# Performance work log

Hardware: AMD Instinct MI355X
Metric: run time of the kernel (lower is better)

The kernel has to match this reference:

```python
import jax, jax.numpy as jnp
import numpy as np

EMBED = 256
HEADS = 8
LEVELS = 4
POINTS = 8
HD = EMBED // HEADS  # 32


def setup_inputs() -> dict:
    key = jax.random.key(0)
    ks = jax.random.split(key, 12)
    bs, nq = 1, 22500
    shapes = np.array([[100, 100], [50, 50], [25, 25], [13, 13]], dtype=np.int32)
    areas = shapes[:, 0] * shapes[:, 1]
    nv = int(areas.sum())  # 13294
    lsi = np.concatenate([[0], np.cumsum(areas)[:-1]]).astype(np.int32)
    s = 1.0 / np.sqrt(EMBED)
    return {
        "query": jax.random.normal(ks[0], (bs, nq, EMBED), jnp.float32),
        "value": jax.random.normal(ks[1], (bs, nv, EMBED), jnp.float32),
        "reference_points": jax.random.uniform(ks[2], (bs, nq, LEVELS, 2), jnp.float32),
        "spatial_shapes": shapes,          # static int metadata
        "level_start_index": lsi,          # static int metadata
        "W_value": jax.random.normal(ks[3], (EMBED, EMBED), jnp.float32) * s,
        "b_value": jax.random.normal(ks[4], (EMBED,), jnp.float32) * 0.01,
        "W_off": jax.random.normal(ks[5], (EMBED, HEADS * LEVELS * POINTS * 2), jnp.float32) * s,
        "b_off": jax.random.normal(ks[6], (HEADS * LEVELS * POINTS * 2,), jnp.float32) * 0.5,
        "W_attn": jax.random.normal(ks[7], (EMBED, HEADS * LEVELS * POINTS), jnp.float32) * s,
        "b_attn": jax.random.normal(ks[8], (HEADS * LEVELS * POINTS,), jnp.float32) * 0.01,
        "W_out": jax.random.normal(ks[9], (EMBED, EMBED), jnp.float32) * s,
        "b_out": jax.random.normal(ks[10], (EMBED,), jnp.float32) * 0.01,
    }


def _bilinear(img, xy):
    # img: (B, H, W, C); xy: (B, N, 2) normalized to [0,1], align_corners=False,
    # zero padding for out-of-range samples (matches F.grid_sample in the torch fallback).
    B, H, W, C = img.shape
    x = xy[..., 0] * W - 0.5
    y = xy[..., 1] * H - 0.5
    x0f = jnp.floor(x)
    y0f = jnp.floor(y)
    wx = (x - x0f)[..., None]
    wy = (y - y0f)[..., None]
    x0 = x0f.astype(jnp.int32)
    y0 = y0f.astype(jnp.int32)
    flat = img.reshape(B, H * W, C)

    def g(yi, xi):
        valid = ((yi >= 0) & (yi < H) & (xi >= 0) & (xi < W)).astype(img.dtype)
        idx = jnp.clip(yi, 0, H - 1) * W + jnp.clip(xi, 0, W - 1)
        return jnp.take_along_axis(flat, idx[..., None], axis=1) * valid[..., None]

    v00 = g(y0, x0)
    v01 = g(y0, x0 + 1)
    v10 = g(y0 + 1, x0)
    v11 = g(y0 + 1, x0 + 1)
    return (v00 * (1 - wy) * (1 - wx) + v01 * (1 - wy) * wx
            + v10 * wy * (1 - wx) + v11 * wy * wx)


def reference(query, value, reference_points, spatial_shapes, level_start_index,
              W_value, b_value, W_off, b_off, W_attn, b_attn, W_out, b_out):
    bs, nq, _ = query.shape
    # value projection -> per-head values (bs, nv, H, hd)
    v = (value @ W_value + b_value).reshape(bs, -1, HEADS, HD)
    # sampling offsets (bs, nq, H, L, P, 2) and attention weights softmaxed over L*P
    off = (query @ W_off + b_off).reshape(bs, nq, HEADS, LEVELS, POINTS, 2)
    aw = jax.nn.softmax((query @ W_attn + b_attn).reshape(bs, nq, HEADS, LEVELS * POINTS), -1)
    aw = aw.reshape(bs, nq, HEADS, LEVELS, POINTS)
    ss = np.asarray(spatial_shapes)
    norm = jnp.asarray(np.stack([ss[:, 1], ss[:, 0]], -1).astype(np.float32))  # (L, 2) as (W, H)
    loc = reference_points[:, :, None, :, None, :] + off / norm[None, None, None, :, None, :]
    out = jnp.zeros((bs, nq, HEADS, HD), query.dtype)
    start = 0
    for l in range(LEVELS):
        H, W = int(ss[l, 0]), int(ss[l, 1])
        vl = v[:, start:start + H * W].reshape(bs, H, W, HEADS, HD)
        vl = vl.transpose(0, 3, 1, 2, 4).reshape(bs * HEADS, H, W, HD)
        ll = loc[:, :, :, l].transpose(0, 2, 1, 3, 4).reshape(bs * HEADS, nq * POINTS, 2)
        samp = _bilinear(vl, ll).reshape(bs, HEADS, nq, POINTS, HD)
        out = out + jnp.einsum('bhqp,bhqpd->bqhd', aw[:, :, :, l].transpose(0, 2, 1, 3), samp)
        start += H * W
    out = out.reshape(bs, nq, EMBED) @ W_out + b_out
    return query + out  # identity residual (identity defaults to query)
```

## Files before the change

### kernel.cpp

```cpp
#include <hip/hip_runtime.h>
#include <hip/hip_bf16.h>
#include <cstdint>

#define NQ 22500
#define NV 13294
#define EMBED 256

typedef short bf16x8 __attribute__((ext_vector_type(8)));
typedef float f32x4  __attribute__((ext_vector_type(4)));

__device__ __forceinline__ int lvlH(int l) { return l==0?100 : l==1?50 : l==2?25 : 13; }
__device__ __forceinline__ int lvlW(int l) { return l==0?100 : l==1?50 : l==2?25 : 13; }
__device__ __forceinline__ int lvlStart(int l) { return l==0?0 : l==1?10000 : l==2?12500 : 13125; }

__device__ __forceinline__ ushort f2bf(float x) {
    uint32_t u = __float_as_uint(x);
    uint32_t r = (u + 0x7FFFu + ((u >> 16) & 1u)) >> 16;
    return (ushort)r;
}

__global__ __launch_bounds__(256) void prep_kernel(
    const float* __restrict__ value, const float* __restrict__ query,
    const float* __restrict__ Wv, const float* __restrict__ Wo,
    const float* __restrict__ Wa, const float* __restrict__ Wt,
    ushort* __restrict__ val_bf, ushort* __restrict__ q_bf,
    ushort* __restrict__ Wv_t, ushort* __restrict__ Wo_t,
    ushort* __restrict__ Wa_t, ushort* __restrict__ Wt_t)
{
    const int y = blockIdx.y;
    const int idx0 = blockIdx.x * 256 + threadIdx.x;
    const int stride = gridDim.x * 256;

    if (y == 0) {
        for (int i = idx0; i < (NV * 256) / 4; i += stride) {
            float4 v = ((const float4*)value)[i];
            ushort4 o; o.x = f2bf(v.x); o.y = f2bf(v.y); o.z = f2bf(v.z); o.w = f2bf(v.w);
            ((ushort4*)val_bf)[i] = o;
        }
    } else if (y == 1) {
        for (int i = idx0; i < (NQ * 256) / 4; i += stride) {
            float4 v = ((const float4*)query)[i];
            ushort4 o; o.x = f2bf(v.x); o.y = f2bf(v.y); o.z = f2bf(v.z); o.w = f2bf(v.w);
            ((ushort4*)q_bf)[i] = o;
        }
    } else if (y == 2) {
        for (int i = idx0; i < 256 * 256; i += stride) {
            int n = i & 255, k = i >> 8;
            Wv_t[n * 256 + k] = f2bf(Wv[k * 256 + n]);
        }
    } else if (y == 3) {
        for (int i = idx0; i < 512 * 256; i += stride) {
            int n = i & 511, k = i >> 9;
            Wo_t[n * 256 + k] = f2bf(Wo[k * 512 + n]);
        }
    } else if (y == 4) {
        for (int i = idx0; i < 256 * 256; i += stride) {
            int n = i & 255, k = i >> 8;
            Wa_t[n * 256 + k] = f2bf(Wa[k * 256 + n]);
        }
    } else {
        for (int i = idx0; i < 256 * 256; i += stride) {
            int n = i & 255, k = i >> 8;
            Wt_t[n * 256 + k] = f2bf(Wt[k * 256 + n]);
        }
    }
}

template<bool RESID>
__global__ __launch_bounds__(256) void gemm_bf16(
    const ushort* __restrict__ A,
    const ushort* __restrict__ Bt,
    const float* __restrict__ bias, const float* __restrict__ R,
    float* __restrict__ C, int M, int N)
{
    __shared__ __align__(16) ushort As[64][40];
    __shared__ __align__(16) ushort Bs[64][40];

    const int tid  = threadIdx.x;
    const int row0 = blockIdx.x * 64;
    const int col0 = blockIdx.y * 64;
    const int wave = tid >> 6, lane = tid & 63;
    const int wm = wave >> 1, wn = wave & 1;
    const int r = lane & 15, g = lane >> 4;
    const int sr = tid >> 2, sc = tid & 3;

    f32x4 acc[2][2] = {};

    const int arow = row0 + sr;
    const bool aok = arow < M;
    const ushort* Aptr = A + (size_t)arow * 256 + sc * 8;
    const ushort* Bptr = Bt + (size_t)(col0 + sr) * 256 + sc * 8;

    for (int k0 = 0; k0 < 256; k0 += 32) {
        uint4 av = aok ? *(const uint4*)(Aptr + k0) : make_uint4(0, 0, 0, 0);
        uint4 bv = *(const uint4*)(Bptr + k0);
        *(uint4*)&As[sr][sc * 8] = av;
        *(uint4*)&Bs[sr][sc * 8] = bv;
        __syncthreads();

        bf16x8 af0 = *(const bf16x8*)&As[wm * 32 + r][g * 8];
        bf16x8 af1 = *(const bf16x8*)&As[wm * 32 + 16 + r][g * 8];
        bf16x8 bf0 = *(const bf16x8*)&Bs[wn * 32 + r][g * 8];
        bf16x8 bf1 = *(const bf16x8*)&Bs[wn * 32 + 16 + r][g * 8];

        acc[0][0] = __builtin_amdgcn_mfma_f32_16x16x32_bf16(af0, bf0, acc[0][0], 0, 0, 0);
        acc[0][1] = __builtin_amdgcn_mfma_f32_16x16x32_bf16(af0, bf1, acc[0][1], 0, 0, 0);
        acc[1][0] = __builtin_amdgcn_mfma_f32_16x16x32_bf16(af1, bf0, acc[1][0], 0, 0, 0);
        acc[1][1] = __builtin_amdgcn_mfma_f32_16x16x32_bf16(af1, bf1, acc[1][1], 0, 0, 0);
        __syncthreads();
    }

#pragma unroll
    for (int mi = 0; mi < 2; ++mi)
#pragma unroll
        for (int ni = 0; ni < 2; ++ni) {
            const int col = col0 + wn * 32 + ni * 16 + r;
            const float bb = bias[col];
#pragma unroll
            for (int j = 0; j < 4; ++j) {
                const int row = row0 + wm * 32 + mi * 16 + g * 4 + j;
                if (row < M) {
                    float o = acc[mi][ni][j] + bb;
                    if (RESID) o += R[(size_t)row * N + col];
                    C[(size_t)row * N + col] = o;
                }
            }
        }
}

__global__ __launch_bounds__(256) void sample_kernel(
    const float* __restrict__ v,
    const float* __restrict__ off_raw,
    const float* __restrict__ attn_raw,
    const float* __restrict__ rp,
    ushort* __restrict__ agg)
{
    __shared__ int4   idxs[8][32];
    __shared__ float4 wts[8][32];

    const int q    = blockIdx.x;
    const int tid  = threadIdx.x;
    const int h    = tid >> 5;
    const int lane = tid & 31;
    const int l    = lane >> 3;
    const int p    = lane & 7;

    const float ox = off_raw[(size_t)q * 512 + h * 64 + l * 16 + p * 2 + 0];
    const float oy = off_raw[(size_t)q * 512 + h * 64 + l * 16 + p * 2 + 1];
    const float rx = rp[(size_t)q * 8 + l * 2 + 0];
    const float ry = rp[(size_t)q * 8 + l * 2 + 1];
    const float Wl = (float)lvlW(l), Hl = (float)lvlH(l);
    const int   Wi = lvlW(l), Hi = lvlH(l), base = lvlStart(l);
    const float xf = rx * Wl + ox - 0.5f;
    const float yf = ry * Hl + oy - 0.5f;

    float logit = attn_raw[(size_t)q * 256 + h * 32 + lane];
    float m = logit;
#pragma unroll
    for (int s = 16; s; s >>= 1) m = fmaxf(m, __shfl_xor(m, s, 32));
    float e = __expf(logit - m);
    float ssum = e;
#pragma unroll
    for (int s = 16; s; s >>= 1) ssum += __shfl_xor(ssum, s, 32);
    const float w = e / ssum;

    const float x0f = floorf(xf), y0f = floorf(yf);
    const float fx = xf - x0f, fy = yf - y0f;
    const int x0 = (int)x0f, y0 = (int)y0f;
    const int x1 = x0 + 1, y1 = y0 + 1;

    const bool vx0 = (unsigned)x0 < (unsigned)Wi;
    const bool vx1 = (unsigned)x1 < (unsigned)Wi;
    const bool vy0 = (unsigned)y0 < (unsigned)Hi;
    const bool vy1 = (unsigned)y1 < (unsigned)Hi;
    const int cx0 = vx0 ? x0 : 0, cx1 = vx1 ? x1 : 0;
    const int cy0 = vy0 ? y0 : 0, cy1 = vy1 ? y1 : 0;

    int4 idx;
    idx.x = base + cy0 * Wi + cx0;
    idx.y = base + cy0 * Wi + cx1;
    idx.z = base + cy1 * Wi + cx0;
    idx.w = base + cy1 * Wi + cx1;
    float4 wv;
    wv.x = (vy0 && vx0) ? w * (1.f - fy) * (1.f - fx) : 0.f;
    wv.y = (vy0 && vx1) ? w * (1.f - fy) * fx         : 0.f;
    wv.z = (vy1 && vx0) ? w * fy * (1.f - fx)         : 0.f;
    wv.w = (vy1 && vx1) ? w * fy * fx                 : 0.f;

    idxs[h][lane] = idx;
    wts[h][lane]  = wv;
    __syncthreads();

    const int slot = lane >> 3;
    const int cg   = lane & 7;
    const float* vbase = v + h * 32 + cg * 4;

    float4 acc = make_float4(0.f, 0.f, 0.f, 0.f);
#pragma unroll
    for (int i = 0; i < 8; ++i) {
        const int s = slot * 8 + i;
        const int4   id = idxs[h][s];
        const float4 ww = wts[h][s];
        const float4 v00 = *(const float4*)(vbase + (size_t)id.x * 256);
        const float4 v01 = *(const float4*)(vbase + (size_t)id.y * 256);
        const float4 v10 = *(const float4*)(vbase + (size_t)id.z * 256);
        const float4 v11 = *(const float4*)(vbase + (size_t)id.w * 256);
        acc.x += ww.x * v00.x + ww.y * v01.x + ww.z * v10.x + ww.w * v11.x;
        acc.y += ww.x * v00.y + ww.y * v01.y + ww.z * v10.y + ww.w * v11.y;
        acc.z += ww.x * v00.z + ww.y * v01.z + ww.z * v10.z + ww.w * v11.z;
        acc.w += ww.x * v00.w + ww.y * v01.w + ww.z * v10.w + ww.w * v11.w;
    }

#pragma unroll
    for (int s = 8; s <= 16; s <<= 1) {
        acc.x += __shfl_xor(acc.x, s, 32);
        acc.y += __shfl_xor(acc.y, s, 32);
        acc.z += __shfl_xor(acc.z, s, 32);
        acc.w += __shfl_xor(acc.w, s, 32);
    }

    if (slot == 0) {
        ushort4 pk;
        pk.x = f2bf(acc.x); pk.y = f2bf(acc.y); pk.z = f2bf(acc.z); pk.w = f2bf(acc.w);
        *(ushort4*)(agg + (size_t)q * 256 + h * 32 + cg * 4) = pk;
    }
}

extern "C" void kernel_launch(void* const* d_in, const int* in_sizes, int n_in,
                              void* d_out, int out_size, void* d_ws, size_t ws_size,
                              hipStream_t stream)
{
    const float* query   = (const float*)d_in[0];
    const float* value   = (const float*)d_in[1];
    const float* rp      = (const float*)d_in[2];
    const float* W_value = (const float*)d_in[5];
    const float* b_value = (const float*)d_in[6];
    const float* W_off   = (const float*)d_in[7];
    const float* b_off   = (const float*)d_in[8];
    const float* W_attn  = (const float*)d_in[9];
    const float* b_attn  = (const float*)d_in[10];
    const float* W_out   = (const float*)d_in[11];
    const float* b_out   = (const float*)d_in[12];
    float* out = (float*)d_out;

    float*  v_ws    = (float*)d_ws;
    float*  off_ws  = v_ws + (size_t)NV * 256;
    float*  attn_ws = off_ws + (size_t)NQ * 512;
    ushort* q_bf    = (ushort*)(attn_ws + (size_t)NQ * 256);
    ushort* val_bf  = q_bf + (size_t)NQ * 256;
    ushort* Wv_t    = val_bf + (size_t)NV * 256;
    ushort* Wo_t    = Wv_t + 256 * 256;
    ushort* Wa_t    = Wo_t + 512 * 256;
    ushort* Wt_t    = Wa_t + 256 * 256;
    ushort* agg_bf  = q_bf;

    dim3 blk(256);

    prep_kernel<<<dim3(2048, 6), blk, 0, stream>>>(
        value, query, W_value, W_off, W_attn, W_out,
        val_bf, q_bf, Wv_t, Wo_t, Wa_t, Wt_t);

    gemm_bf16<false><<<dim3((NV + 63) / 64, 4), blk, 0, stream>>>(
        val_bf, Wv_t, b_value, nullptr, v_ws, NV, 256);
    gemm_bf16<false><<<dim3((NQ + 63) / 64, 8), blk, 0, stream>>>(
        q_bf, Wo_t, b_off, nullptr, off_ws, NQ, 512);
    gemm_bf16<false><<<dim3((NQ + 63) / 64, 4), blk, 0, stream>>>(
        q_bf, Wa_t, b_attn, nullptr, attn_ws, NQ, 256);
    sample_kernel<<<NQ, blk, 0, stream>>>(v_ws, off_ws, attn_ws, rp, agg_bf);
    gemm_bf16<true><<<dim3((NQ + 63) / 64, 4), blk, 0, stream>>>(
        agg_bf, Wt_t, b_out, query, out, NQ, 256);
}
```

Measured before the change: 296.1 us.

## Store projected value in bf16 and enlarge GEMM tiles to 128x64 with K=64

The value projection GEMM now writes bf16 instead of fp32, and the sampling kernel gathers 8 bf16 channels per lane with 16-byte loads. Each lane now covers a sampling-point slot and the reduction runs across slots. This halves the bytes moved by the random bilinear gathers, at the cost of lower precision in the sampled values. Separately, the GEMM tile grows to 128x64 with a 64-wide K step and 8 MFMAs per wave per substep, which improves reuse and halves the number of barriers.

Measured after the change: 342.9 us. 15.8% more time.

```diff
diff --git a/kernel.cpp b/kernel.cpp
--- a/kernel.cpp
+++ b/kernel.cpp
@@ -66,70 +66,103 @@
     }
 }
 
-template<bool RESID>
+template<bool RESID, bool OUT_BF16>
 __global__ __launch_bounds__(256) void gemm_bf16(
     const ushort* __restrict__ A,
     const ushort* __restrict__ Bt,
     const float* __restrict__ bias, const float* __restrict__ R,
-    float* __restrict__ C, int M, int N)
+    void* __restrict__ Cv, int M, int N)
 {
-    __shared__ __align__(16) ushort As[64][40];
-    __shared__ __align__(16) ushort Bs[64][40];
+    __shared__ __align__(16) ushort As[128][72];
+    __shared__ __align__(16) ushort Bs[64][72];
 
     const int tid  = threadIdx.x;
-    const int row0 = blockIdx.x * 64;
+    const int row0 = blockIdx.x * 128;
     const int col0 = blockIdx.y * 64;
     const int wave = tid >> 6, lane = tid & 63;
-    const int wm = wave >> 1, wn = wave & 1;
     const int r = lane & 15, g = lane >> 4;
-    const int sr = tid >> 2, sc = tid & 3;
-
-    f32x4 acc[2][2] = {};
-
-    const int arow = row0 + sr;
-    const bool aok = arow < M;
-    const ushort* Aptr = A + (size_t)arow * 256 + sc * 8;
-    const ushort* Bptr = Bt + (size_t)(col0 + sr) * 256 + sc * 8;
-
-    for (int k0 = 0; k0 < 256; k0 += 32) {
-        uint4 av = aok ? *(const uint4*)(Aptr + k0) : make_uint4(0, 0, 0, 0);
-        uint4 bv = *(const uint4*)(Bptr + k0);
-        *(uint4*)&As[sr][sc * 8] = av;
-        *(uint4*)&Bs[sr][sc * 8] = bv;
+
+    const int ar = tid >> 1, ac = (tid & 1) * 32;
+    const int br = tid >> 2, bc = (tid & 3) * 16;
+    const bool aok = (row0 + ar) < M;
+    const ushort* Aptr = A + (size_t)(row0 + ar) * 256 + ac;
+    const ushort* Bptr = Bt + (size_t)(col0 + br) * 256 + bc;
+
+    f32x4 acc[2][4] = {};
+
+    for (int k0 = 0; k0 < 256; k0 += 64) {
+        uint4 av[4], bv[2];
+#pragma unroll
+        for (int j = 0; j < 4; ++j)
+            av[j] = aok ? *(const uint4*)(Aptr + k0 + j * 8) : make_uint4(0, 0, 0, 0);
+#pragma unroll
+        for (int j = 0; j < 2; ++j)
+            bv[j] = *(const uint4*)(Bptr + k0 + j * 8);
+
+#pragma unroll
+        for (int j = 0; j < 4; ++j)
+            *(uint4*)&As[ar][ac + j * 8] = av[j];
+#pragma unroll
+        for (int j = 0; j < 2; ++j)
+            *(uint4*)&Bs[br][bc + j * 8] = bv[j];
         __syncthreads();
 
-        bf16x8 af0 = *(const bf16x8*)&As[wm * 32 + r][g * 8];
-        bf16x8 af1 = *(const bf16x8*)&As[wm * 32 + 16 + r][g * 8];
-        bf16x8 bf0 = *(const bf16x8*)&Bs[wn * 32 + r][g * 8];
-        bf16x8 bf1 = *(const bf16x8*)&Bs[wn * 32 + 16 + r][g * 8];
-
-        acc[0][0] = __builtin_amdgcn_mfma_f32_16x16x32_bf16(af0, bf0, acc[0][0], 0, 0, 0);
-        acc[0][1] = __builtin_amdgcn_mfma_f32_16x16x32_bf16(af0, bf1, acc[0][1], 0, 0, 0);
-        acc[1][0] = __builtin_amdgcn_mfma_f32_16x16x32_bf16(af1, bf0, acc[1][0], 0, 0, 0);
-        acc[1][1] = __builtin_amdgcn_mfma_f32_16x16x32_bf16(af1, bf1, acc[1][1], 0, 0, 0);
+#pragma unroll
+        for (int kk = 0; kk < 2; ++kk) {
+            const int kc = kk * 32 + g * 8;
+            bf16x8 a0 = *(const bf16x8*)&As[wave * 32 + r][kc];
+            bf16x8 a1 = *(const bf16x8*)&As[wave * 32 + 16 + r][kc];
+            bf16x8 b0 = *(const bf16x8*)&Bs[r][kc];
+            bf16x8 b1 = *(const bf16x8*)&Bs[16 + r][kc];
+            bf16x8 b2 = *(const bf16x8*)&Bs[32 + r][kc];
+            bf16x8 b3 = *(const bf16x8*)&Bs[48 + r][kc];
+
+            acc[0][0] = __builtin_amdgcn_mfma_f32_16x16x32_bf16(a0, b0, acc[0][0], 0, 0, 0);
+            acc[0][1] = __builtin_amdgcn_mfma_f32_16x16x32_bf16(a0, b1, acc[0][1], 0, 0, 0);
+            acc[0][2] = __builtin_amdgcn_mfma_f32_16x16x32_bf16(a0, b2, acc[0][2], 0, 0, 0);
+            acc[0][3] = __builtin_amdgcn_mfma_f32_16x16x32_bf16(a0, b3, acc[0][3], 0, 0, 0);
+            acc[1][0] = __builtin_amdgcn_mfma_f32_16x16x32_bf16(a1, b0, acc[1][0], 0, 0, 0);
+            acc[1][1] = __builtin_amdgcn_mfma_f32_16x16x32_bf16(a1, b1, acc[1][1], 0, 0, 0);
+            acc[1][2] = __builtin_amdgcn_mfma_f32_16x16x32_bf16(a1, b2, acc[1][2], 0, 0, 0);
+            acc[1][3] = __builtin_amdgcn_mfma_f32_16x16x32_bf16(a1, b3, acc[1][3], 0, 0, 0);
+        }
         __syncthreads();
     }
 
 #pragma unroll
     for (int mi = 0; mi < 2; ++mi)
 #pragma unroll
-        for (int ni = 0; ni < 2; ++ni) {
-            const int col = col0 + wn * 32 + ni * 16 + r;
+        for (int ni = 0; ni < 4; ++ni) {
+            const int col = col0 + ni * 16 + r;
             const float bb = bias[col];
 #pragma unroll
             for (int j = 0; j < 4; ++j) {
-                const int row = row0 + wm * 32 + mi * 16 + g * 4 + j;
+                const int row = row0 + wave * 32 + mi * 16 + g * 4 + j;
                 if (row < M) {
                     float o = acc[mi][ni][j] + bb;
                     if (RESID) o += R[(size_t)row * N + col];
-                    C[(size_t)row * N + col] = o;
+                    if (OUT_BF16)
+                        ((ushort*)Cv)[(size_t)row * N + col] = f2bf(o);
+                    else
+                        ((float*)Cv)[(size_t)row * N + col] = o;
                 }
             }
         }
 }
 
+__device__ __forceinline__ void fma8(float* acc, uint4 u, float w) {
+    acc[0] += w * __uint_as_float(u.x << 16);
+    acc[1] += w * __uint_as_float(u.x & 0xffff0000u);
+    acc[2] += w * __uint_as_float(u.y << 16);
+    acc[3] += w * __uint_as_float(u.y & 0xffff0000u);
+    acc[4] += w * __uint_as_float(u.z << 16);
+    acc[5] += w * __uint_as_float(u.z & 0xffff0000u);
+    acc[6] += w * __uint_as_float(u.w << 16);
+    acc[7] += w * __uint_as_float(u.w & 0xffff0000u);
+}
+
 __global__ __launch_bounds__(256) void sample_kernel(
-    const float* __restrict__ v,
+    const ushort* __restrict__ v,
     const float* __restrict__ off_raw,
     const float* __restrict__ attn_raw,
     const float* __restrict__ rp,
@@ -191,38 +224,37 @@
     wts[h][lane]  = wv;
     __syncthreads();
 
-    const int slot = lane >> 3;
-    const int cg   = lane & 7;
-    const float* vbase = v + h * 32 + cg * 4;
-
-    float4 acc = make_float4(0.f, 0.f, 0.f, 0.f);
-#pragma unroll
-    for (int i = 0; i < 8; ++i) {
-        const int s = slot * 8 + i;
+    const int slot = lane & 7;
+    const int cg   = lane >> 3;
+    const ushort* vbase = v + h * 32 + cg * 8;
+
+    float acc[8] = {};
+#pragma unroll
+    for (int i = 0; i < 4; ++i) {
+        const int s = slot + i * 8;
         const int4   id = idxs[h][s];
         const float4 ww = wts[h][s];
-        const float4 v00 = *(const float4*)(vbase + (size_t)id.x * 256);
-        const float4 v01 = *(const float4*)(vbase + (size_t)id.y * 256);
-        const float4 v10 = *(const float4*)(vbase + (size_t)id.z * 256);
-        const float4 v11 = *(const float4*)(vbase + (size_t)id.w * 256);
-        acc.x += ww.x * v00.x + ww.y * v01.x + ww.z * v10.x + ww.w * v11.x;
-        acc.y += ww.x * v00.y + ww.y * v01.y + ww.z * v10.y + ww.w * v11.y;
-        acc.z += ww.x * v00.z + ww.y * v01.z + ww.z * v10.z + ww.w * v11.z;
-        acc.w += ww.x * v00.w + ww.y * v01.w + ww.z * v10.w + ww.w * v11.w;
+        uint4 c00 = *(const uint4*)(vbase + (size_t)id.x * 256);
+        uint4 c01 = *(const uint4*)(vbase + (size_t)id.y * 256);
+        uint4 c10 = *(const uint4*)(vbase + (size_t)id.z * 256);
+        uint4 c11 = *(const uint4*)(vbase + (size_t)id.w * 256);
+        fma8(acc, c00, ww.x);
+        fma8(acc, c01, ww.y);
+        fma8(acc, c10, ww.z);
+        fma8(acc, c11, ww.w);
     }
 
 #pragma unroll
-    for (int s = 8; s <= 16; s <<= 1) {
-        acc.x += __shfl_xor(acc.x, s, 32);
-        acc.y += __shfl_xor(acc.y, s, 32);
-        acc.z += __shfl_xor(acc.z, s, 32);
-        acc.w += __shfl_xor(acc.w, s, 32);
-    }
+    for (int m8 = 1; m8 <= 4; m8 <<= 1)
+#pragma unroll
+        for (int j = 0; j < 8; ++j)
+            acc[j] += __shfl_xor(acc[j], m8, 32);
 
     if (slot == 0) {
-        ushort4 pk;
-        pk.x = f2bf(acc.x); pk.y = f2bf(acc.y); pk.z = f2bf(acc.z); pk.w = f2bf(acc.w);
-        *(ushort4*)(agg + (size_t)q * 256 + h * 32 + cg * 4) = pk;
+        ushort pk[8];
+#pragma unroll
+        for (int j = 0; j < 8; ++j) pk[j] = f2bf(acc[j]);
+        *(uint4*)(agg + (size_t)q * 256 + h * 32 + cg * 8) = *(const uint4*)pk;
     }
 }
 
@@ -243,8 +275,8 @@
     const float* b_out   = (const float*)d_in[12];
     float* out = (float*)d_out;
 
-    float*  v_ws    = (float*)d_ws;
-    float*  off_ws  = v_ws + (size_t)NV * 256;
+    ushort* v_bf    = (ushort*)d_ws;
+    float*  off_ws  = (float*)(v_bf + (size_t)NV * 256);
     float*  attn_ws = off_ws + (size_t)NQ * 512;
     ushort* q_bf    = (ushort*)(attn_ws + (size_t)NQ * 256);
     ushort* val_bf  = q_bf + (size_t)NQ * 256;
@@ -260,13 +292,13 @@
         value, query, W_value, W_off, W_attn, W_out,
         val_bf, q_bf, Wv_t, Wo_t, Wa_t, Wt_t);
 
-    gemm_bf16<false><<<dim3((NV + 63) / 64, 4), blk, 0, stream>>>(
-        val_bf, Wv_t, b_value, nullptr, v_ws, NV, 256);
-    gemm_bf16<false><<<dim3((NQ + 63) / 64, 8), blk, 0, stream>>>(
+    gemm_bf16<false, true><<<dim3((NV + 127) / 128, 4), blk, 0, stream>>>(
+        val_bf, Wv_t, b_value, nullptr, v_bf, NV, 256);
+    gemm_bf16<false, false><<<dim3((NQ + 127) / 128, 8), blk, 0, stream>>>(
         q_bf, Wo_t, b_off, nullptr, off_ws, NQ, 512);
-    gemm_bf16<false><<<dim3((NQ + 63) / 64, 4), blk, 0, stream>>>(
+    gemm_bf16<false, false><<<dim3((NQ + 127) / 128, 4), blk, 0, stream>>>(
         q_bf, Wa_t, b_attn, nullptr, attn_ws, NQ, 256);
-    sample_kernel<<<NQ, blk, 0, stream>>>(v_ws, off_ws, attn_ws, rp, agg_bf);
-    gemm_bf16<true><<<dim3((NQ + 63) / 64, 4), blk, 0, stream>>>(
+    sample_kernel<<<NQ, blk, 0, stream>>>(v_bf, off_ws, attn_ws, rp, agg_bf);
+    gemm_bf16<true, false><<<dim3((NQ + 127) / 128, 4), blk, 0, stream>>>(
         agg_bf, Wt_t, b_out, query, out, NQ, 256);
 }
```
